# Kernel tuning notes

Measured on AMD Instinct MI355X. Metric: run time of the kernel, lower is better.

The kernel has to match this reference:

```python
import jax, jax.numpy as jnp
import numpy as np

B, N, D = 2, 2048, 1024
H, HD = 16, 64
SCALE = HD ** (-0.5)


def setup_inputs() -> dict:
    key = jax.random.key(0)
    k1, k2, k3, k4 = jax.random.split(key, 4)
    x = jax.random.normal(k1, (B, N, D), dtype=jnp.float32)
    mask = jax.random.randint(k2, (B, 1, N, N), 0, 2) == 1  # bool, True = masked out
    W_qkv = jax.random.normal(k3, (D, 3 * H * HD), dtype=jnp.float32) * (D ** -0.5)
    W_out = jax.random.normal(k4, (H * HD, D), dtype=jnp.float32) * ((H * HD) ** -0.5)
    b_out = jnp.zeros((D,), dtype=jnp.float32)
    return {"x": x, "mask": mask, "W_qkv": W_qkv, "W_out": W_out, "b_out": b_out}


def reference(x, mask, W_qkv, W_out, b_out):
    b, n, _ = x.shape
    qkv = x @ W_qkv                                  # [b, n, 3*h*hd]
    q, k, v = jnp.split(qkv, 3, axis=-1)
    split_heads = lambda t: t.reshape(b, n, H, HD).transpose(0, 2, 1, 3)  # b h n d
    q, k, v = split_heads(q), split_heads(k), split_heads(v)
    scores = jnp.einsum('bhid,bhjd->bhij', q, k) * SCALE
    scores = jnp.where(mask, jnp.finfo(scores.dtype).min, scores)
    attn = jax.nn.softmax(scores, axis=-1)           # dropout p=0 -> identity
    out = jnp.einsum('bhij,bhjd->bhid', attn, v)     # [b, h, n, hd]
    out = out.transpose(0, 2, 1, 3).reshape(b, n, H * HD)
    return out @ W_out + b_out
```

## Files before the change

### kernel.cpp

```cpp
#include <hip/hip_runtime.h>
#include <stdint.h>

typedef unsigned short u16;
typedef short short8 __attribute__((ext_vector_type(8)));
typedef float f32x4 __attribute__((ext_vector_type(4)));
typedef float f32x16 __attribute__((ext_vector_type(16)));
typedef unsigned int uint2v __attribute__((ext_vector_type(2)));

#define K2E 0.18033688011112042f

__device__ __forceinline__ u16 f2bf(float f) {
  union { float f; uint32_t u; } v;
  v.f = f;
  uint32_t u = v.u;
  u += 0x7FFFu + ((u >> 16) & 1u);
  return (u16)(u >> 16);
}

__device__ __forceinline__ uint32_t cvtpk(float lo, float hi) {
  uint32_t r;
  asm("v_cvt_pk_bf16_f32 %0, %1, %2" : "=v"(r) : "v"(lo), "v"(hi));
  return r;
}

__device__ __forceinline__ float exp2a(float x) {
  float r;
  asm("v_exp_f32 %0, %1" : "=v"(r) : "v"(x));
  return r;
}

__device__ __forceinline__ float mask_zero(float p, uint32_t zm, int oc) {
  int mext = __builtin_amdgcn_sbfe((int)zm, oc, 1);
  float r;
  asm("v_bfi_b32 %0, %1, 0, %2" : "=v"(r) : "v"(mext), "v"(p));
  return r;
}

__device__ __forceinline__ void gld_lds16(const u16* src, char* dst) {
  __builtin_amdgcn_global_load_lds((const __attribute__((address_space(1))) void*)src,
                                   (__attribute__((address_space(3))) void*)dst, 16, 0, 0);
}

__device__ __forceinline__ void pack_frags(const f32x16& v, short8& fa, short8& fb) {
  union U { uint32_t w[4]; short8 v8; };
  uint32_t X0 = cvtpk(v[0], v[1]),   X1 = cvtpk(v[2], v[3]);
  uint32_t Y0 = cvtpk(v[4], v[5]),   Y1 = cvtpk(v[6], v[7]);
  uint32_t X2 = cvtpk(v[8], v[9]),   X3 = cvtpk(v[10], v[11]);
  uint32_t Y2 = cvtpk(v[12], v[13]), Y3 = cvtpk(v[14], v[15]);
  uint2v r0 = __builtin_amdgcn_permlane32_swap(X0, Y0, false, false);
  uint2v r1 = __builtin_amdgcn_permlane32_swap(X1, Y1, false, false);
  uint2v r2 = __builtin_amdgcn_permlane32_swap(X2, Y2, false, false);
  uint2v r3 = __builtin_amdgcn_permlane32_swap(X3, Y3, false, false);
  U ua; ua.w[0] = r0.x; ua.w[1] = r1.x; ua.w[2] = r0.y; ua.w[3] = r1.y; fa = ua.v8;
  U ub; ub.w[0] = r2.x; ub.w[1] = r3.x; ub.w[2] = r2.y; ub.w[3] = r3.y; fb = ub.v8;
}

__global__ __launch_bounds__(256) void k_prep(const float* __restrict__ x,
                                              u16* __restrict__ xb,
                                              const float* __restrict__ Wqkv,
                                              u16* __restrict__ wqT,
                                              const float* __restrict__ Wout,
                                              u16* __restrict__ woT,
                                              const int* __restrict__ m,
                                              uint32_t* __restrict__ mw) {
  __shared__ float tsh[32][33];
  const int bid = blockIdx.x;
  const int t = threadIdx.x;
  if (bid < 4096) {
    int g = bid * 256 + t;
    float4 v = ((const float4*)x)[g];
    ushort4 o;
    o.x = f2bf(v.x); o.y = f2bf(v.y); o.z = f2bf(v.z); o.w = f2bf(v.w);
    ((ushort4*)xb)[g] = o;
  } else if (bid < 8192) {
    const float* src; u16* dst; int R, C, bb;
    if (bid < 7168) { src = Wqkv; dst = wqT; R = 1024; C = 3072; bb = bid - 4096;
    } else           { src = Wout; dst = woT; R = 1024; C = 1024; bb = bid - 7168; }
    const int nbx = C >> 5;
    const int c0 = (bb % nbx) * 32, r0 = (bb / nbx) * 32;
    const int tx = t & 31, ty = t >> 5;
#pragma unroll
    for (int i = 0; i < 4; ++i)
      tsh[ty + 8 * i][tx] = src[(size_t)(r0 + ty + 8 * i) * C + c0 + tx];
    __syncthreads();
#pragma unroll
    for (int i = 0; i < 4; ++i)
      dst[(size_t)(c0 + ty + 8 * i) * R + r0 + tx] = f2bf(tsh[tx][ty + 8 * i]);
  } else {
    int g = (bid - 8192) * 256 + t;
    unsigned long long bal = __ballot(m[g] != 0);
    int lane = t & 63;
    if (lane == 0) mw[g >> 5] = (uint32_t)bal;
    else if (lane == 32) mw[g >> 5] = (uint32_t)(bal >> 32);
  }
}


#define GS(U, BUF)                                                   \
  {                                                                  \
    char* dA_ = lds + (BUF) * 16384 + (w << 11);                     \
    const u16* a_ = As + ((U) << 5);                                 \
    const u16* b_ = Bs + ((U) << 5);                                 \
    gld_lds16(a_, dA_);                                              \
    gld_lds16(a_ + (K << 4), dA_ + 1024);                            \
    gld_lds16(b_, dA_ + 8192);                                       \
    gld_lds16(b_ + (K << 4), dA_ + 9216);                            \
  }

#define PH(U, BUF, DOSTAGE, VMS)                                                          \
  {                                                                                       \
    asm volatile("s_waitcnt vmcnt(" VMS ")" ::: "memory");                                \
    __builtin_amdgcn_sched_barrier(0);                                                    \
    __builtin_amdgcn_s_barrier();                                                         \
    __builtin_amdgcn_sched_barrier(0);                                                    \
    const char* rb_ = lds + (BUF) * 16384;                                                \
    short8 af[4], bfr[4];                                                                 \
    _Pragma("unroll")                                                                     \
    for (int mi = 0; mi < 4; ++mi) {                                                      \
      int row = wm * 64 + mi * 16 + lr;                                                   \
      af[mi] = *(const short8*)(rb_ + row * 64 + ((lg ^ ((row >> 1) & 3)) << 4));         \
    }                                                                                     \
    _Pragma("unroll")                                                                     \
    for (int ni = 0; ni < 4; ++ni) {                                                      \
      int row = wn * 64 + ni * 16 + lr;                                                   \
      bfr[ni] = *(const short8*)(rb_ + 8192 + row * 64 + ((lg ^ ((row >> 1) & 3)) << 4)); \
    }                                                                                     \
    asm volatile("s_waitcnt lgkmcnt(0)" ::: "memory");                                    \
    __builtin_amdgcn_sched_barrier(0);                                                    \
    __builtin_amdgcn_s_barrier();                                                         \
    __builtin_amdgcn_sched_barrier(0);                                                    \
    if (DOSTAGE) GS((U) + 3, BUF);                                                        \
    __builtin_amdgcn_s_setprio(1);                                                        \
    _Pragma("unroll")                                                                     \
    for (int mi = 0; mi < 4; ++mi)                                                        \
      _Pragma("unroll")                                                                   \
      for (int ni = 0; ni < 4; ++ni)                                                      \
        acc[mi][ni] =                                                                     \
            __builtin_amdgcn_mfma_f32_16x16x32_bf16(af[mi], bfr[ni], acc[mi][ni], 0, 0, 0); \
    __builtin_amdgcn_s_setprio(0);                                                        \
  }

__device__ __forceinline__ void gemm_core(const u16* __restrict__ A,
                                          const u16* __restrict__ Bt,
                                          int K, int m0, int n0,
                                          f32x4 (&acc)[4][4], char* lds) {
  const int t = threadIdx.x;
  const int l = t & 63;
  const int w = t >> 6;
  const int wm = w >> 1, wn = w & 1;
  const int lr = l & 15, lg = l >> 4;
  const int r0 = (w << 5) + (l >> 2);
  const int c = (l & 3) ^ ((r0 >> 1) & 3);
  const u16* As = A + (size_t)(m0 + r0) * K + c * 8;
  const u16* Bs = Bt + (size_t)(n0 + r0) * K + c * 8;

  GS(0, 0);
  GS(1, 1);
  GS(2, 2);

#pragma unroll 1
  for (int i = 0; i < 9; ++i) {
    const int u = 3 * i;
    PH(u + 0, 0, true, "8");
    PH(u + 1, 1, true, "8");
    PH(u + 2, 2, true, "8");
  }
  PH(27, 0, true, "8");
  PH(28, 1, true, "8");
  PH(29, 2, false, "8");
  PH(30, 0, false, "4");
  PH(31, 1, false, "0");
}

__global__ __launch_bounds__(256, 3) void k_gemm_qkv(const u16* __restrict__ xb,
                                                     const u16* __restrict__ wqT,
                                                     u16* __restrict__ Qb,
                                                     u16* __restrict__ Kb,
                                                     u16* __restrict__ VT) {
  __shared__ char lds[49152] __attribute__((aligned(128)));
  const int bid = blockIdx.x;
  const int wg = (bid & 7) * 96 + (bid >> 3);
  const int m0 = (wg / 24) * 128, n0 = (wg % 24) * 128;
  f32x4 acc[4][4] = {};
  gemm_core(xb, wqT, 1024, m0, n0, acc, lds);
  const int l = threadIdx.x & 63, w = threadIdx.x >> 6;
  const int wm = w >> 1, wn = w & 1;
  const int lr = l & 15, lg = l >> 4;
#pragma unroll
  for (int mi = 0; mi < 4; ++mi)
#pragma unroll
    for (int ni = 0; ni < 4; ++ni)
#pragma unroll
      for (int r = 0; r < 4; ++r) {
        int m = m0 + wm * 64 + mi * 16 + lg * 4 + r;
        int n = n0 + wn * 64 + ni * 16 + lr;
        int b = m >> 11, seq = m & 2047;
        float av = acc[mi][ni][r];
        if (n < 1024) {
          Qb[((size_t)((b << 4) + (n >> 6)) * 2048 + seq) * 64 + (n & 63)] = f2bf(av * K2E);
        } else if (n < 2048) {
          int nn = n - 1024;
          Kb[((size_t)((b << 4) + (nn >> 6)) * 2048 + seq) * 64 + (nn & 63)] = f2bf(av);
        } else {
          int nn = n - 2048;
          VT[((size_t)((b << 4) + (nn >> 6)) * 64 + (nn & 63)) * 2048 + seq] = f2bf(av);
        }
      }
}

__global__ __launch_bounds__(256, 3) void k_gemm_out(const u16* __restrict__ ao,
                                                     const u16* __restrict__ woT,
                                                     const float* __restrict__ bias,
                                                     float* __restrict__ out) {
  __shared__ char lds[49152] __attribute__((aligned(128)));
  const int bid = blockIdx.x;
  const int wg = (bid & 7) * 32 + (bid >> 3);
  const int m0 = (wg >> 3) * 128, n0 = (wg & 7) * 128;
  f32x4 acc[4][4] = {};
  gemm_core(ao, woT, 1024, m0, n0, acc, lds);
  const int l = threadIdx.x & 63, w = threadIdx.x >> 6;
  const int wm = w >> 1, wn = w & 1;
  const int lr = l & 15, lg = l >> 4;
#pragma unroll
  for (int mi = 0; mi < 4; ++mi)
#pragma unroll
    for (int ni = 0; ni < 4; ++ni)
#pragma unroll
      for (int r = 0; r < 4; ++r) {
        int m = m0 + wm * 64 + mi * 16 + lg * 4 + r;
        int n = n0 + wn * 64 + ni * 16 + lr;
        out[(size_t)m * 1024 + n] = acc[mi][ni][r] + bias[n];
      }
}

__global__ __launch_bounds__(512, 4) void k_attn(const u16* __restrict__ Qg,
                                                 const u16* __restrict__ Kg,
                                                 const u16* __restrict__ Vg,
                                                 const uint32_t* __restrict__ maskw,
                                                 u16* __restrict__ AO) {
  __shared__ char lds[65536] __attribute__((aligned(128)));
  const int bid0 = blockIdx.x;
  const int bid = (bid0 & 7) * 64 + (bid0 >> 3);
  const int qt = bid & 15;
  const int hd = (bid >> 4) & 15;
  const int b = bid >> 8;
  const int bh = (b << 4) + hd;
  const int tx = threadIdx.x, l = tx & 63, w = tx >> 6;
  const int wq = w & 3, kvh = w >> 2;
  const int l31 = l & 31, h = l >> 5;
  const int hx4 = (h ^ (l & 7)) << 4;
  const int sc8 = ((l & 7) ^ (l >> 3)) << 3;
  const int lr8 = l >> 3;

  const u16* Qp = Qg + (size_t)bh * 131072;
  const int q = qt * 128 + wq * 32 + l31;
  const int kv0 = kvh << 10;

  const u16* kg = Kg + (size_t)bh * 131072 + (size_t)(kv0 + 16 * wq + lr8) * 64 + sc8;
  const u16* vg = Vg + (size_t)bh * 131072 + (size_t)(16 * wq + lr8) * 2048 + kv0 + sc8;
  const uint2v* mp = (const uint2v*)(maskw + ((size_t)(b << 11) + q) * 64) + (kvh << 4);

  short8 qf[4];
#pragma unroll
  for (int s = 0; s < 4; ++s)
    qf[s] = *(const short8*)(Qp + (size_t)q * 64 + s * 16 + h * 8);

  const short8 ones8 = {0x3F80, 0x3F80, 0x3F80, 0x3F80, 0x3F80, 0x3F80, 0x3F80, 0x3F80};
  f32x16 Oa[2] = {};
  f32x16 acc_l = {};
  char* ldsH = lds + (kvh << 15);

#define STAGE(BSEL, TT)                                       \
  {                                                           \
    char* base_ = ldsH + (BSEL) * 16384 + (wq << 11);         \
    const u16* k_ = kg + ((size_t)(TT) << 12);                \
    const u16* v_ = vg + ((size_t)(TT) << 6);                 \
    gld_lds16(k_, base_);                                     \
    gld_lds16(k_ + 512, base_ + 1024);                        \
    gld_lds16(v_, base_ + 8192);                              \
    gld_lds16(v_ + 16384, base_ + 9216);                      \
  }

  STAGE(0, 0);

#pragma unroll 1
  for (int tt = 0; tt < 16; ++tt) {
    __syncthreads();
    if (tt + 1 < 16) STAGE((tt + 1) & 1, tt + 1);
    const uint2v mm = mp[tt];
    const char* kbase = ldsH + (tt & 1) * 16384 + l31 * 128;
    const char* vbase = kbase + 8192;

    f32x16 sa = {}, sb = {};
    __builtin_amdgcn_s_setprio(1);
#pragma unroll
    for (int s = 0; s < 4; ++s) {
      short8 k0 = *(const short8*)(kbase + ((s << 5) ^ hx4));
      short8 k1 = *(const short8*)(kbase + 4096 + ((s << 5) ^ hx4));
      sa = __builtin_amdgcn_mfma_f32_32x32x16_bf16(k0, qf[s], sa, 0, 0, 0);
      sb = __builtin_amdgcn_mfma_f32_32x32x16_bf16(k1, qf[s], sb, 0, 0, 0);
    }
    __builtin_amdgcn_s_setprio(0);

    const uint32_t zm0 = mm.x >> (4 * h);
    const uint32_t zm1 = mm.y >> (4 * h);
#pragma unroll
    for (int r = 0; r < 16; ++r) {
      const int oc = (r & 3) + 8 * (r >> 2);
      sa[r] = mask_zero(exp2a(sa[r]), zm0, oc);
      sb[r] = mask_zero(exp2a(sb[r]), zm1, oc);
    }

    short8 pf[4];
    pack_frags(sa, pf[0], pf[1]);
    pack_frags(sb, pf[2], pf[3]);

    __builtin_amdgcn_s_setprio(1);
#pragma unroll
    for (int cc = 0; cc < 4; ++cc) {
      short8 v0 = *(const short8*)(vbase + ((cc << 5) ^ hx4));
      short8 v1 = *(const short8*)(vbase + 4096 + ((cc << 5) ^ hx4));
      Oa[0] = __builtin_amdgcn_mfma_f32_32x32x16_bf16(v0, pf[cc], Oa[0], 0, 0, 0);
      Oa[1] = __builtin_amdgcn_mfma_f32_32x32x16_bf16(v1, pf[cc], Oa[1], 0, 0, 0);
      acc_l = __builtin_amdgcn_mfma_f32_32x32x16_bf16(ones8, pf[cc], acc_l, 0, 0, 0);
    }
    __builtin_amdgcn_s_setprio(0);
  }
#undef STAGE

  __syncthreads();
  float* cb = (float*)lds;
  if (kvh) {
#pragma unroll
    for (int r = 0; r < 32; ++r)
      cb[((wq << 5) + r) * 64 + l] = Oa[r >> 4][r & 15];
    cb[8192 + (wq << 6) + l] = acc_l[0];
  }
  __syncthreads();
  if (!kvh) {
#pragma unroll
    for (int r = 0; r < 32; ++r)
      Oa[r >> 4][r & 15] += cb[((wq << 5) + r) * 64 + l];
    float lt = acc_l[0] + cb[8192 + (wq << 6) + l];
    float inv = 1.0f / fmaxf(lt, 1e-30f);
    u16* orow = AO + ((size_t)(b << 11) + q) * 1024 + hd * 64 + h * 4;
#pragma unroll
    for (int dt = 0; dt < 2; ++dt)
#pragma unroll
      for (int rq = 0; rq < 4; ++rq) {
        uint32_t w0 = cvtpk(Oa[dt][4 * rq + 0] * inv, Oa[dt][4 * rq + 1] * inv);
        uint32_t w1 = cvtpk(Oa[dt][4 * rq + 2] * inv, Oa[dt][4 * rq + 3] * inv);
        *(uint32_t*)(orow + dt * 32 + rq * 8) = w0;
        *(uint32_t*)(orow + dt * 32 + rq * 8 + 2) = w1;
      }
  }
}


extern "C" void kernel_launch(void* const* d_in, const int* in_sizes, int n_in,
                              void* d_out, int out_size, void* d_ws, size_t ws_size,
                              hipStream_t stream) {
  const float* x = (const float*)d_in[0];
  const int* mask = (const int*)d_in[1];
  const float* Wqkv = (const float*)d_in[2];
  const float* Wout = (const float*)d_in[3];
  const float* bout = (const float*)d_in[4];
  float* out = (float*)d_out;
  char* ws = (char*)d_ws;
  const size_t MB = 1u << 20;
  if (ws_size < 49 * MB) return;

  u16* xb = (u16*)(ws);
  u16* wqT = (u16*)(ws + 8 * MB);
  u16* woT = (u16*)(ws + 14 * MB);
  uint32_t* mw = (uint32_t*)(ws + 16 * MB);
  u16* Qb = (u16*)(ws + 17 * MB);
  u16* Kb = (u16*)(ws + 25 * MB);
  u16* VT = (u16*)(ws + 33 * MB);
  u16* AO = (u16*)(ws + 41 * MB);

  k_prep<<<40960, 256, 0, stream>>>(x, xb, Wqkv, wqT, Wout, woT, mask, mw);
  k_gemm_qkv<<<768, 256, 0, stream>>>(xb, wqT, Qb, Kb, VT);
  k_attn<<<512, 512, 0, stream>>>(Qb, Kb, VT, mw, AO);
  k_gemm_out<<<256, 256, 0, stream>>>(AO, woT, bout, out);
}
```

Before: 129.2 us.

## Stage V-transpose through LDS and use 64x128 tiles for output GEMM

The QKV GEMM epilogue for the V columns now transposes the tile through LDS and writes VT with coalesced 16-byte stores instead of strided scalar u16 stores. The output projection GEMM switches from 128x128 tiles over 256 blocks to 64x128 tiles over 512 blocks, with a dedicated triple-buffered pipeline and smaller LDS so more blocks fit per CU. This is meant to fix uncoalesced VT writes and the under-filled grid on the output GEMM. The cost is an extra LDS round trip and barriers in the V epilogue, and less operand reuse per block in the output GEMM.

```diff
diff --git a/kernel.cpp b/kernel.cpp
--- a/kernel.cpp
+++ b/kernel.cpp
@@ -127,7 +127,7 @@
     }                                                                                     \
     asm volatile("s_waitcnt lgkmcnt(0)" ::: "memory");                                    \
     __builtin_amdgcn_sched_barrier(0);                                                    \
-    __builtin_amdgcn_s_barrier();                                                         \
+    __builtin_amdgcn_s_barrier();                                                        \
     __builtin_amdgcn_sched_barrier(0);                                                    \
     if (DOSTAGE) GS((U) + 3, BUF);                                                        \
     __builtin_amdgcn_s_setprio(1);                                                        \
@@ -186,48 +186,139 @@
   const int l = threadIdx.x & 63, w = threadIdx.x >> 6;
   const int wm = w >> 1, wn = w & 1;
   const int lr = l & 15, lg = l >> 4;
-#pragma unroll
-  for (int mi = 0; mi < 4; ++mi)
-#pragma unroll
-    for (int ni = 0; ni < 4; ++ni)
-#pragma unroll
-      for (int r = 0; r < 4; ++r) {
-        int m = m0 + wm * 64 + mi * 16 + lg * 4 + r;
-        int n = n0 + wn * 64 + ni * 16 + lr;
-        int b = m >> 11, seq = m & 2047;
-        float av = acc[mi][ni][r];
-        if (n < 1024) {
-          Qb[((size_t)((b << 4) + (n >> 6)) * 2048 + seq) * 64 + (n & 63)] = f2bf(av * K2E);
-        } else if (n < 2048) {
-          int nn = n - 1024;
-          Kb[((size_t)((b << 4) + (nn >> 6)) * 2048 + seq) * 64 + (nn & 63)] = f2bf(av);
-        } else {
-          int nn = n - 2048;
-          VT[((size_t)((b << 4) + (nn >> 6)) * 64 + (nn & 63)) * 2048 + seq] = f2bf(av);
+  const int b = m0 >> 11;
+  if (n0 >= 2048) {
+    __syncthreads();
+    u16* lt = (u16*)lds;
+#pragma unroll
+    for (int mi = 0; mi < 4; ++mi)
+#pragma unroll
+      for (int ni = 0; ni < 4; ++ni)
+#pragma unroll
+        for (int r = 0; r < 4; ++r) {
+          int ml = wm * 64 + mi * 16 + lg * 4 + r;
+          int nl = wn * 64 + ni * 16 + lr;
+          lt[nl * 136 + ml] = f2bf(acc[mi][ni][r]);
         }
-      }
-}
-
-__global__ __launch_bounds__(256, 3) void k_gemm_out(const u16* __restrict__ ao,
+    __syncthreads();
+    const int nl = threadIdx.x >> 1, hf = threadIdx.x & 1;
+    const int nn = n0 - 2048 + nl;
+    const int seq = (m0 & 2047) + hf * 64;
+    u16* dst = VT + ((size_t)((b << 4) + (nn >> 6)) * 64 + (nn & 63)) * 2048 + seq;
+    const u16* srcr = lt + nl * 136 + hf * 64;
+#pragma unroll
+    for (int i = 0; i < 8; ++i)
+      *(uint4*)(dst + i * 8) = *(const uint4*)(srcr + i * 8);
+  } else {
+#pragma unroll
+    for (int mi = 0; mi < 4; ++mi)
+#pragma unroll
+      for (int ni = 0; ni < 4; ++ni)
+#pragma unroll
+        for (int r = 0; r < 4; ++r) {
+          int m = m0 + wm * 64 + mi * 16 + lg * 4 + r;
+          int n = n0 + wn * 64 + ni * 16 + lr;
+          int seq = m & 2047;
+          float av = acc[mi][ni][r];
+          if (n < 1024) {
+            Qb[((size_t)((b << 4) + (n >> 6)) * 2048 + seq) * 64 + (n & 63)] = f2bf(av * K2E);
+          } else {
+            int nn = n - 1024;
+            Kb[((size_t)((b << 4) + (nn >> 6)) * 2048 + seq) * 64 + (nn & 63)] = f2bf(av);
+          }
+        }
+  }
+}
+
+
+#define OGS(U, BUF)                                                  \
+  {                                                                  \
+    char* d_ = lds + (BUF) * 12288 + (w << 10);                      \
+    const u16* a_ = As + ((U) << 5);                                 \
+    const u16* b_ = Bs + ((U) << 5);                                 \
+    gld_lds16(a_, d_);                                               \
+    gld_lds16(b_, d_ + 4096);                                        \
+    gld_lds16(b_ + (K << 6), d_ + 8192);                             \
+  }
+
+#define OPH(U, BUF, DOSTAGE, VMS)                                                         \
+  {                                                                                       \
+    asm volatile("s_waitcnt vmcnt(" VMS ")" ::: "memory");                                \
+    __builtin_amdgcn_sched_barrier(0);                                                    \
+    __builtin_amdgcn_s_barrier();                                                         \
+    __builtin_amdgcn_sched_barrier(0);                                                    \
+    const char* rb_ = lds + (BUF) * 12288;                                                \
+    short8 af[2], bfr[4];                                                                 \
+    _Pragma("unroll")                                                                     \
+    for (int mi = 0; mi < 2; ++mi) {                                                      \
+      int row = wm * 32 + mi * 16 + lr;                                                   \
+      af[mi] = *(const short8*)(rb_ + row * 64 + ((lg ^ ((row >> 1) & 3)) << 4));         \
+    }                                                                                     \
+    _Pragma("unroll")                                                                     \
+    for (int ni = 0; ni < 4; ++ni) {                                                      \
+      int row = wn * 64 + ni * 16 + lr;                                                   \
+      bfr[ni] = *(const short8*)(rb_ + 4096 + row * 64 + ((lg ^ ((row >> 1) & 3)) << 4)); \
+    }                                                                                     \
+    asm volatile("s_waitcnt lgkmcnt(0)" ::: "memory");                                    \
+    __builtin_amdgcn_sched_barrier(0);                                                    \
+    __builtin_amdgcn_s_barrier();                                                        \
+    __builtin_amdgcn_sched_barrier(0);                                                    \
+    if (DOSTAGE) OGS((U) + 3, BUF);                                                       \
+    __builtin_amdgcn_s_setprio(1);                                                        \
+    _Pragma("unroll")                                                                     \
+    for (int mi = 0; mi < 2; ++mi)                                                        \
+      _Pragma("unroll")                                                                   \
+      for (int ni = 0; ni < 4; ++ni)                                                      \
+        acc[mi][ni] =                                                                     \
+            __builtin_amdgcn_mfma_f32_16x16x32_bf16(af[mi], bfr[ni], acc[mi][ni], 0, 0, 0); \
+    __builtin_amdgcn_s_setprio(0);                                                        \
+  }
+
+__global__ __launch_bounds__(256, 4) void k_gemm_out(const u16* __restrict__ ao,
                                                      const u16* __restrict__ woT,
                                                      const float* __restrict__ bias,
                                                      float* __restrict__ out) {
-  __shared__ char lds[49152] __attribute__((aligned(128)));
+  __shared__ char lds[36864] __attribute__((aligned(128)));
+  const int K = 1024;
   const int bid = blockIdx.x;
-  const int wg = (bid & 7) * 32 + (bid >> 3);
-  const int m0 = (wg >> 3) * 128, n0 = (wg & 7) * 128;
-  f32x4 acc[4][4] = {};
-  gemm_core(ao, woT, 1024, m0, n0, acc, lds);
-  const int l = threadIdx.x & 63, w = threadIdx.x >> 6;
+  const int wg = (bid & 7) * 64 + (bid >> 3);
+  const int m0 = (wg >> 3) * 64, n0 = (wg & 7) * 128;
+  const int t = threadIdx.x;
+  const int l = t & 63;
+  const int w = t >> 6;
   const int wm = w >> 1, wn = w & 1;
   const int lr = l & 15, lg = l >> 4;
-#pragma unroll
-  for (int mi = 0; mi < 4; ++mi)
+  const int sr = (w << 4) + (l >> 2);
+  const int sc = (l & 3) ^ ((sr >> 1) & 3);
+  const u16* As = ao + (size_t)(m0 + sr) * K + sc * 8;
+  const u16* Bs = woT + (size_t)(n0 + sr) * K + sc * 8;
+
+  f32x4 acc[2][4] = {};
+
+  OGS(0, 0);
+  OGS(1, 1);
+  OGS(2, 2);
+
+#pragma unroll 1
+  for (int i = 0; i < 9; ++i) {
+    const int u = 3 * i;
+    OPH(u + 0, 0, true, "6");
+    OPH(u + 1, 1, true, "6");
+    OPH(u + 2, 2, true, "6");
+  }
+  OPH(27, 0, true, "6");
+  OPH(28, 1, true, "6");
+  OPH(29, 2, false, "6");
+  OPH(30, 0, false, "3");
+  OPH(31, 1, false, "0");
+
+#pragma unroll
+  for (int mi = 0; mi < 2; ++mi)
 #pragma unroll
     for (int ni = 0; ni < 4; ++ni)
 #pragma unroll
       for (int r = 0; r < 4; ++r) {
-        int m = m0 + wm * 64 + mi * 16 + lg * 4 + r;
+        int m = m0 + wm * 32 + mi * 16 + lg * 4 + r;
         int n = n0 + wn * 64 + ni * 16 + lr;
         out[(size_t)m * 1024 + n] = acc[mi][ni][r] + bias[n];
       }
@@ -382,5 +473,5 @@
   k_prep<<<40960, 256, 0, stream>>>(x, xb, Wqkv, wqT, Wout, woT, mask, mw);
   k_gemm_qkv<<<768, 256, 0, stream>>>(xb, wqT, Qb, Kb, VT);
   k_attn<<<512, 512, 0, stream>>>(Qb, Kb, VT, mw, AO);
-  k_gemm_out<<<256, 256, 0, stream>>>(AO, woT, bout, out);
-}
+  k_gemm_out<<<512, 256, 0, stream>>>(AO, woT, bout, out);
+}
```

Result: faster. 125.8 us (median of 3 runs) (-2.6%).
